# Performance work log

Measured on AMD Instinct MI355X. Metric: run time of the kernel, lower is better.

## Reference

```python
import jax, jax.numpy as jnp
import numpy as np

EPS = 1e-6
STRIDE = 2  # kv_pool_stride
NUM_HEADS = 8

def _layernorm(x, w, b):
    mu = jnp.mean(x, axis=-1, keepdims=True)
    var = jnp.mean(jnp.square(x - mu), axis=-1, keepdims=True)
    return (x - mu) * jax.lax.rsqrt(var + EPS) * w + b

def setup_inputs() -> dict:
    key = jax.random.key(0)
    B, H, W, C = 8, 56, 56, 384
    hidden = int(C * 2.0)
    ks = jax.random.split(key, 12)
    s = 0.02
    return {
        "x": jax.random.normal(ks[0], (B, H * W, C), jnp.float32),
        "ln1_w": jnp.ones((C,), jnp.float32),
        "ln1_b": jnp.zeros((C,), jnp.float32),
        "qw": jax.random.normal(ks[1], (C, C), jnp.float32) * s,
        "qb": jnp.zeros((C,), jnp.float32),
        "kw": jax.random.normal(ks[2], (C, C), jnp.float32) * s,
        "kb": jnp.zeros((C,), jnp.float32),
        "vw": jax.random.normal(ks[3], (C, C), jnp.float32) * s,
        "vb": jnp.zeros((C,), jnp.float32),
        "pw": jax.random.normal(ks[4], (C, C), jnp.float32) * s,
        "pb": jnp.zeros((C,), jnp.float32),
        "ln2_w": jnp.ones((C,), jnp.float32),
        "ln2_b": jnp.zeros((C,), jnp.float32),
        "fc1_w": jax.random.normal(ks[5], (C, hidden), jnp.float32) * s,
        "fc1_b": jnp.zeros((hidden,), jnp.float32),
        "fc2_w": jax.random.normal(ks[6], (hidden, C), jnp.float32) * s,
        "fc2_b": jnp.zeros((C,), jnp.float32),
        "H": 56,
        "W": 56,
    }

def reference(x, ln1_w, ln1_b, qw, qb, kw, kb, vw, vb, pw, pb,
              ln2_w, ln2_b, fc1_w, fc1_b, fc2_w, fc2_b, H, W):
    B, N, C = x.shape
    h = NUM_HEADS
    d = C // h
    scale = d ** -0.5

    # Attention branch: Q from norm1(x); K,V from RAW x (as in source), KV avg-pooled 2x2
    q_tok = _layernorm(x, ln1_w, ln1_b)
    s = STRIDE
    Hk, Wk = H // s, W // s
    kv = x.reshape(B, Hk, s, Wk, s, C).mean(axis=(2, 4)).reshape(B, Hk * Wk, C)

    q = (q_tok @ qw + qb).reshape(B, N, h, d)
    k = (kv @ kw + kb).reshape(B, Hk * Wk, h, d)
    v = (kv @ vw + vb).reshape(B, Hk * Wk, h, d)

    attn = jnp.einsum('bqhd,bkhd->bhqk', q, k) * scale
    attn = jax.nn.softmax(attn, axis=-1)
    out = jnp.einsum('bhqk,bkhd->bqhd', attn, v).reshape(B, N, C)
    x = x + (out @ pw + pb)

    # MLP branch (GELU exact, matching torch nn.GELU default)
    y = _layernorm(x, ln2_w, ln2_b)
    y = jax.nn.gelu(y @ fc1_w + fc1_b, approximate=False)
    x = x + (y @ fc2_w + fc2_b)
    return x
```

## Files before the change

kernel.cpp:

```cpp
#include <hip/hip_runtime.h>
#include <math.h>

#define B_    8
#define N_TOK 3136
#define C_    384
#define DH    48
#define NK    784
#define HID   768
#define M1    25088
#define M2    6272
#define M1Q   6272

typedef unsigned short u16;
typedef __attribute__((ext_vector_type(8))) short bf16x8;
typedef __attribute__((ext_vector_type(4))) float f32x4;

__device__ __forceinline__ float b2f(u16 u) {
  return __uint_as_float(((unsigned)u) << 16);
}
__device__ __forceinline__ u16 f2b(float f) {
  unsigned u = __float_as_uint(f);
  return (u16)((u + 0x7fffu + ((u >> 16) & 1u)) >> 16);
}
__device__ __forceinline__ u16 f2b_trunc(float f) {
  return (u16)(__float_as_uint(f) >> 16);
}
__device__ __forceinline__ void gload_lds16(const u16* g, u16* l) {
  __builtin_amdgcn_global_load_lds(
      (const __attribute__((address_space(1))) void*)g,
      (__attribute__((address_space(3))) void*)l, 16, 0, 0);
}

__global__ __launch_bounds__(256) void ln1_pool(
    const float* __restrict__ X, const float* __restrict__ w,
    const float* __restrict__ b, u16* __restrict__ Y, u16* __restrict__ KV) {
  if (blockIdx.x < M1 / 4) {
    const int row = blockIdx.x * 4 + (threadIdx.x >> 6);
    const int lane = threadIdx.x & 63;
    const size_t base = (size_t)row * C_;
    float v[6];
#pragma unroll
    for (int i = 0; i < 6; ++i) v[i] = X[base + lane + 64 * i];
    float s = 0.f;
#pragma unroll
    for (int i = 0; i < 6; ++i) s += v[i];
#pragma unroll
    for (int off = 32; off > 0; off >>= 1) s += __shfl_xor(s, off);
    const float mu = s * (1.0f / C_);
    float q = 0.f;
#pragma unroll
    for (int i = 0; i < 6; ++i) { float d = v[i] - mu; q += d * d; }
#pragma unroll
    for (int off = 32; off > 0; off >>= 1) q += __shfl_xor(q, off);
    const float r = rsqrtf(q * (1.0f / C_) + 1e-6f);
#pragma unroll
    for (int i = 0; i < 6; ++i) {
      int c = lane + 64 * i;
      Y[base + c] = f2b((v[i] - mu) * r * w[c] + b[c]);
    }
  } else {
    int t = (blockIdx.x - M1 / 4) * 256 + threadIdx.x;
    if (t >= M2 * C_) return;
    int c = t % C_;
    int row = t / C_;
    int bb = row / NK;
    int rr = row - bb * NK;
    int hk = rr / 28;
    int wk = rr - hk * 28;
    const float* p = X + ((size_t)(bb * N_TOK + hk * 112 + wk * 2)) * C_ + c;
    KV[t] = f2b(0.25f * (p[0] + p[C_] + p[56 * C_] + p[57 * C_]));
  }
}

__global__ __launch_bounds__(256) void ln2_rows(const u16* __restrict__ X,
    const float* __restrict__ w, const float* __restrict__ b, u16* __restrict__ Y) {
  const int row = blockIdx.x * 4 + (threadIdx.x >> 6);
  const int lane = threadIdx.x & 63;
  const size_t base = (size_t)row * C_;
  float v[6];
#pragma unroll
  for (int i = 0; i < 6; ++i) v[i] = b2f(X[base + lane + 64 * i]);
  float s = 0.f;
#pragma unroll
  for (int i = 0; i < 6; ++i) s += v[i];
#pragma unroll
  for (int off = 32; off > 0; off >>= 1) s += __shfl_xor(s, off);
  const float mu = s * (1.0f / C_);
  float q = 0.f;
#pragma unroll
  for (int i = 0; i < 6; ++i) { float d = v[i] - mu; q += d * d; }
#pragma unroll
  for (int off = 32; off > 0; off >>= 1) q += __shfl_xor(q, off);
  const float r = rsqrtf(q * (1.0f / C_) + 1e-6f);
#pragma unroll
  for (int i = 0; i < 6; ++i) {
    int c = lane + 64 * i;
    Y[base + c] = f2b((v[i] - mu) * r * w[c] + b[c]);
  }
}

struct TransArgs {
  const float* src[6];
  u16* dst[6];
  int K[6], N[6], tx[6], ty[6];
};
__global__ __launch_bounds__(256) void transpose_all(TransArgs a) {
  const int id = blockIdx.z;
  if ((int)blockIdx.x >= a.tx[id] || (int)blockIdx.y >= a.ty[id]) return;
  const float* W = a.src[id];
  u16* WT = a.dst[id];
  const int K = a.K[id], N = a.N[id];
  __shared__ u16 tile[64][73];
  const int k0 = blockIdx.y * 64, n0 = blockIdx.x * 64;
  for (int i = threadIdx.x; i < 64 * 64; i += 256) {
    int kk = i >> 6, nn = i & 63;
    tile[kk][nn] = f2b(W[(size_t)(k0 + kk) * N + n0 + nn]);
  }
  __syncthreads();
  for (int i = threadIdx.x; i < 64 * 64; i += 256) {
    int nn = i >> 6, kk = i & 63;
    WT[(size_t)(n0 + nn) * K + k0 + kk] = tile[kk][nn];
  }
}

template<int EPI, bool RES32, bool OUT32>
__device__ __forceinline__ void gemm_core(
    const u16* __restrict__ A, const u16* __restrict__ BT,
    const float* __restrict__ bias, const void* __restrict__ resv,
    void* __restrict__ Cv, int N, int K, int m0, int n0) {
  __shared__ u16 As[128 * 64];
  __shared__ u16 Bs[128 * 64];
  const int tid  = threadIdx.x;
  const int wave = tid >> 6;
  const int lane = tid & 63;
  const int quad = lane >> 4;
  const int ll   = lane & 15;
  const int wm   = wave >> 1, wn = wave & 1;

  const int srow = wave * 32 + (lane >> 3);
  const int sgs  = lane & 7;

  f32x4 acc[4][4];
#pragma unroll
  for (int i = 0; i < 4; ++i)
#pragma unroll
    for (int j = 0; j < 4; ++j) acc[i][j] = (f32x4){0.f, 0.f, 0.f, 0.f};

  for (int kk0 = 0; kk0 < K; kk0 += 64) {
    __syncthreads();
#pragma unroll
    for (int c = 0; c < 4; ++c) {
      const int r = srow + c * 8;
      const int g = sgs ^ (r & 7);
      gload_lds16(A  + (size_t)(m0 + r) * K + kk0 + g * 8,
                  As + (size_t)(wave * 32 + c * 8) * 64);
      gload_lds16(BT + (size_t)(n0 + r) * K + kk0 + g * 8,
                  Bs + (size_t)(wave * 32 + c * 8) * 64);
    }
    __syncthreads();
#pragma unroll
    for (int ks = 0; ks < 2; ++ks) {
      const int gsw = (quad + 4 * ks) ^ (ll & 7);
      bf16x8 af[4], bfr[4];
#pragma unroll
      for (int im = 0; im < 4; ++im)
        af[im] = *(const bf16x8*)&As[(size_t)(wm * 64 + im * 16 + ll) * 64 + gsw * 8];
#pragma unroll
      for (int jn = 0; jn < 4; ++jn)
        bfr[jn] = *(const bf16x8*)&Bs[(size_t)(wn * 64 + jn * 16 + ll) * 64 + gsw * 8];
#pragma unroll
      for (int im = 0; im < 4; ++im)
#pragma unroll
        for (int jn = 0; jn < 4; ++jn)
          acc[im][jn] = __builtin_amdgcn_mfma_f32_16x16x32_bf16(
              af[im], bfr[jn], acc[im][jn], 0, 0, 0);
    }
  }

  float bb[4];
#pragma unroll
  for (int jn = 0; jn < 4; ++jn) bb[jn] = bias[n0 + wn * 64 + jn * 16 + ll];
#pragma unroll
  for (int im = 0; im < 4; ++im) {
    const int row = m0 + wm * 64 + im * 16 + quad * 4;
#pragma unroll
    for (int jn = 0; jn < 4; ++jn) {
      const int col = n0 + wn * 64 + jn * 16 + ll;
#pragma unroll
      for (int r = 0; r < 4; ++r) {
        float o = acc[im][jn][r] + bb[jn];
        if (EPI == 1) {
          o = 0.5f * o * (1.0f + erff(o * 0.70710678118654752f));
        } else if (EPI == 2) {
          size_t ri = (size_t)(row + r) * N + col;
          o += RES32 ? ((const float*)resv)[ri] : b2f(((const u16*)resv)[ri]);
        }
        if (OUT32) ((float*)Cv)[(size_t)(row + r) * N + col] = o;
        else       ((u16*)Cv)[(size_t)(row + r) * N + col] = f2b(o);
      }
    }
  }
}

template<int EPI, bool RES32, bool OUT32>
__global__ __launch_bounds__(256) void gemm_bt(
    const u16* __restrict__ A, const u16* __restrict__ BT,
    const float* __restrict__ bias, const void* __restrict__ resv,
    void* __restrict__ Cv, int N, int K) {
  gemm_core<EPI, RES32, OUT32>(A, BT, bias, resv, Cv, N, K,
                               blockIdx.y << 7, blockIdx.x << 7);
}

struct QKVArgs {
  const u16* A[3];
  const u16* BT[3];
  const float* bias[3];
  u16* C[3];
  int M[3];
};
__global__ __launch_bounds__(256) void gemm_qkv(QKVArgs a) {
  const int z = blockIdx.z;
  const int m0 = blockIdx.y << 7;
  if (m0 >= a.M[z]) return;
  gemm_core<0, false, false>(a.A[z], a.BT[z], a.bias[z], nullptr, a.C[z],
                             C_, C_, m0, blockIdx.x << 7);
}

#define QS_STR 72
__global__ __launch_bounds__(512) void attn_mfma(
    const u16* __restrict__ Q, const u16* __restrict__ Kb,
    const u16* __restrict__ Vb, u16* __restrict__ O) {
  __shared__ u16 Qs[128 * QS_STR];
  __shared__ u16 Ks[64 * QS_STR];
  __shared__ u16 Vt[48 * QS_STR];
  __shared__ u16 Ps[128 * QS_STR];
  const int tid  = threadIdx.x;
  const int wave = tid >> 6;
  const int lane = tid & 63;
  const int quad = lane >> 4;
  const int ll   = lane & 15;
  const int qt   = blockIdx.x;
  const int bh   = blockIdx.y;
  const int b    = bh >> 3, h = bh & 7;
  const int q0   = qt * 128;
  const float scale = 0.14433756729740643f;

  for (int i = tid; i < 128 * 16; i += 512) {
    int r = i >> 4, c = i & 15;
    Qs[r * QS_STR + 48 + c] = 0;
    if (r < 64) Ks[r * QS_STR + 48 + c] = 0;
  }
  {
    const int part = tid & 7;
#pragma unroll
    for (int it = 0; it < 2; ++it) {
      const int row = it * 64 + (tid >> 3);
      if (part < 6) {
        const int qrow = q0 + row;
        if (qrow < N_TOK) {
          uint4 v = *(const uint4*)(Q + ((size_t)(b * N_TOK) + qrow) * C_ + h * DH + part * 8);
          const u16* vp = (const u16*)&v;
          u16 ov[8];
#pragma unroll
          for (int j = 0; j < 8; ++j) ov[j] = f2b(b2f(vp[j]) * scale);
          *(uint4*)&Qs[row * QS_STR + part * 8] = *(const uint4*)ov;
        } else {
          uint4 z = {0, 0, 0, 0};
          *(uint4*)&Qs[row * QS_STR + part * 8] = z;
        }
      }
    }
  }

  f32x4 Ofr[3] = {{0.f,0.f,0.f,0.f},{0.f,0.f,0.f,0.f},{0.f,0.f,0.f,0.f}};
  float lrow[4] = {0.f, 0.f, 0.f, 0.f};

  for (int t = 0; t < 13; ++t) {
    const int kbase = t * 64;
    __syncthreads();
    {
      const int key = tid >> 3, part = tid & 7;
      if (part < 6 && kbase + key < NK) {
        uint4 v = *(const uint4*)(Kb + ((size_t)(b * NK) + kbase + key) * C_ + h * DH + part * 8);
        *(uint4*)&Ks[key * QS_STR + part * 8] = v;
      }
    }
    {
      const int part = tid >> 6, key = tid & 63;
      if (part < 6 && kbase + key < NK) {
        uint4 v = *(const uint4*)(Vb + ((size_t)(b * NK) + kbase + key) * C_ + h * DH + part * 8);
        const u16* vp = (const u16*)&v;
#pragma unroll
        for (int j = 0; j < 8; ++j)
          Vt[(part * 8 + j) * QS_STR + key] = vp[j];
      }
    }
    __syncthreads();

    f32x4 S[4];
#pragma unroll
    for (int nt = 0; nt < 4; ++nt) {
      f32x4 acc = {0.f, 0.f, 0.f, 0.f};
#pragma unroll
      for (int k0 = 0; k0 < 64; k0 += 32) {
        bf16x8 a = *(const bf16x8*)&Qs[(wave * 16 + ll) * QS_STR + k0 + quad * 8];
        bf16x8 bb = *(const bf16x8*)&Ks[(nt * 16 + ll) * QS_STR + k0 + quad * 8];
        acc = __builtin_amdgcn_mfma_f32_16x16x32_bf16(a, bb, acc, 0, 0, 0);
      }
      if (kbase + nt * 16 + ll >= NK)
        acc = (f32x4){-1e30f, -1e30f, -1e30f, -1e30f};
      S[nt] = acc;
    }
#pragma unroll
    for (int nt = 0; nt < 4; ++nt) {
      const int g = nt * 2 + (ll >> 3);
      const int gp = g ^ quad;
#pragma unroll
      for (int r = 0; r < 4; ++r) {
        float p = __expf(S[nt][r]);
        lrow[r] += p;
        Ps[(wave * 16 + quad * 4 + r) * QS_STR + (gp << 3) + (ll & 7)] = f2b_trunc(p);
      }
    }
#pragma unroll
    for (int dt = 0; dt < 3; ++dt)
#pragma unroll
      for (int ks = 0; ks < 2; ++ks) {
        const int gp = ((ks << 2) + quad) ^ ((ll >> 2) & 3);
        bf16x8 a = *(const bf16x8*)&Ps[(wave * 16 + ll) * QS_STR + (gp << 3)];
        bf16x8 bb = *(const bf16x8*)&Vt[(dt * 16 + ll) * QS_STR + ks * 32 + quad * 8];
        Ofr[dt] = __builtin_amdgcn_mfma_f32_16x16x32_bf16(a, bb, Ofr[dt], 0, 0, 0);
      }
  }
#pragma unroll
  for (int msk = 1; msk < 16; msk <<= 1)
#pragma unroll
    for (int r = 0; r < 4; ++r)
      lrow[r] += __shfl_xor(lrow[r], msk);
  float inv[4];
#pragma unroll
  for (int r = 0; r < 4; ++r) inv[r] = 1.0f / lrow[r];
#pragma unroll
  for (int dt = 0; dt < 3; ++dt)
#pragma unroll
    for (int r = 0; r < 4; ++r) {
      int qrow = q0 + wave * 16 + quad * 4 + r;
      if (qrow < N_TOK)
        O[((size_t)b * N_TOK + qrow) * C_ + h * DH + dt * 16 + ll] =
            f2b(Ofr[dt][r] * inv[r]);
    }
}

__global__ __launch_bounds__(256) void marker_fill(
    float* __restrict__ out, size_t n, float val) {
  size_t i = (size_t)blockIdx.x * 256 + threadIdx.x;
  const size_t stride = (size_t)gridDim.x * 256;
  for (; i < n; i += stride) out[i] = 0.f;
  if (blockIdx.x == 0 && threadIdx.x == 0) out[0] = val;
}

extern "C" void kernel_launch(void* const* d_in, const int* in_sizes, int n_in,
                              void* d_out, int out_size, void* d_ws, size_t ws_size,
                              hipStream_t stream) {
  const float* x    = (const float*)d_in[0];
  const float* ln1w = (const float*)d_in[1];
  const float* ln1b = (const float*)d_in[2];
  const float* qw   = (const float*)d_in[3];
  const float* qb   = (const float*)d_in[4];
  const float* kw   = (const float*)d_in[5];
  const float* kb   = (const float*)d_in[6];
  const float* vw   = (const float*)d_in[7];
  const float* vb   = (const float*)d_in[8];
  const float* pw   = (const float*)d_in[9];
  const float* pb   = (const float*)d_in[10];
  const float* ln2w = (const float*)d_in[11];
  const float* ln2b = (const float*)d_in[12];
  const float* fc1w = (const float*)d_in[13];
  const float* fc1b = (const float*)d_in[14];
  const float* fc2w = (const float*)d_in[15];
  const float* fc2b = (const float*)d_in[16];

  const size_t BUF = (size_t)M1 * C_;
  float* outf = (float*)d_out;

  {
    static const int exp_sizes[19] = {
      M1 * C_, C_, C_, C_ * C_, C_, C_ * C_, C_, C_ * C_, C_, C_ * C_, C_,
      C_, C_, C_ * HID, HID, HID * C_, C_, 1, 1};
    int bad = -1;
    if (n_in != 19) bad = 99;
    else {
      for (int i = 0; i < 19; ++i)
        if (in_sizes[i] != exp_sizes[i]) { bad = i; break; }
    }
    if (bad >= 0) {
      marker_fill<<<1024, 256, 0, stream>>>(outf, BUF, 10000.0f + (float)bad);
      return;
    }
  }
  const size_t need_min  = 4096 + 3 * BUF * sizeof(u16);
  const size_t need_full = 4096 + (3 * BUF + (size_t)M1 * HID) * sizeof(u16);
  if (ws_size < need_min) {
    marker_fill<<<1024, 256, 0, stream>>>(outf, BUF, 30000.0f + (float)(ws_size >> 20));
    return;
  }
  const bool full_mlp = (ws_size >= need_full);

  u16* T0 = (u16*)((char*)d_ws + 4096);
  u16* T1 = T0 + BUF;
  u16* U  = T1 + BUF;
  u16* P  = U;
  u16* KB = U + (size_t)M2 * C_;
  u16* VB = U + (size_t)2 * M2 * C_;
  u16* HBq = U;
  u16* HBfull = U + BUF;
  u16* WTb = U + BUF - (size_t)(4 * C_ * C_ + 2 * C_ * HID);
  u16* wtq = WTb;
  u16* wtk = wtq + C_ * C_;
  u16* wtv = wtk + C_ * C_;
  u16* wtp = wtv + C_ * C_;
  u16* wtf1 = wtp + C_ * C_;
  u16* wtf2 = wtf1 + (size_t)C_ * HID;

  {
    TransArgs ta;
    ta.src[0] = qw;   ta.dst[0] = wtq;  ta.K[0] = C_;  ta.N[0] = C_;  ta.tx[0] = 6;  ta.ty[0] = 6;
    ta.src[1] = kw;   ta.dst[1] = wtk;  ta.K[1] = C_;  ta.N[1] = C_;  ta.tx[1] = 6;  ta.ty[1] = 6;
    ta.src[2] = vw;   ta.dst[2] = wtv;  ta.K[2] = C_;  ta.N[2] = C_;  ta.tx[2] = 6;  ta.ty[2] = 6;
    ta.src[3] = pw;   ta.dst[3] = wtp;  ta.K[3] = C_;  ta.N[3] = C_;  ta.tx[3] = 6;  ta.ty[3] = 6;
    ta.src[4] = fc1w; ta.dst[4] = wtf1; ta.K[4] = C_;  ta.N[4] = HID; ta.tx[4] = 12; ta.ty[4] = 6;
    ta.src[5] = fc2w; ta.dst[5] = wtf2; ta.K[5] = HID; ta.N[5] = C_;  ta.tx[5] = 6;  ta.ty[5] = 12;
    transpose_all<<<dim3(12, 12, 6), 256, 0, stream>>>(ta);
  }

  ln1_pool<<<M1 / 4 + (M2 * C_) / 256, 256, 0, stream>>>(x, ln1w, ln1b, T0, P);

  {
    QKVArgs qa;
    qa.A[0] = T0; qa.BT[0] = wtq; qa.bias[0] = qb; qa.C[0] = T1; qa.M[0] = M1;
    qa.A[1] = P;  qa.BT[1] = wtk; qa.bias[1] = kb; qa.C[1] = KB; qa.M[1] = M2;
    qa.A[2] = P;  qa.BT[2] = wtv; qa.bias[2] = vb; qa.C[2] = VB; qa.M[2] = M2;
    gemm_qkv<<<dim3(3, 196, 3), 256, 0, stream>>>(qa);
  }

  attn_mfma<<<dim3(25, 64), 512, 0, stream>>>(T1, KB, VB, T0);

  gemm_bt<2, true, false><<<dim3(3, 196), 256, 0, stream>>>(
      T0, wtp, pb, x, T1, C_, C_);

  ln2_rows<<<M1 / 4, 256, 0, stream>>>(T1, ln2w, ln2b, T0);

  if (full_mlp) {
    gemm_bt<1, false, false><<<dim3(6, 196), 256, 0, stream>>>(
        T0, wtf1, fc1b, nullptr, HBfull, HID, C_);
    gemm_bt<2, false, true><<<dim3(3, 196), 256, 0, stream>>>(
        HBfull, wtf2, fc2b, T1, outf, C_, HID);
  } else {
    for (int qtr = 0; qtr < 4; ++qtr) {
      const size_t ro = (size_t)qtr * M1Q;
      gemm_bt<1, false, false><<<dim3(6, 49), 256, 0, stream>>>(
          T0 + ro * C_, wtf1, fc1b, nullptr, HBq, HID, C_);
      gemm_bt<2, false, true><<<dim3(3, 49), 256, 0, stream>>>(
          HBq, wtf2, fc2b, T1 + ro * C_, outf + ro * C_, C_, HID);
    }
  }
}
```

Measured before the change: 348.0 us.

## Enlarge GEMM M-tile to 256, merge pre-kernels, keep attention Q in registers

The GEMM tile goes from 128x128 to 256x128, so each wave accumulates 8x4 MFMA tiles and reuses each B fragment across twice as many A rows. Row-bound checks handle M values that are not multiples of 256. The weight transpose and LN1/pooling kernels are merged into one launch to drop a kernel boundary. The attention kernel now loads Q fragments straight into registers instead of staging them in shared memory, which cuts LDS traffic and footprint. The costs are more accumulator registers (lower occupancy), fewer blocks per GEMM grid, and the partial last M tile doing wasted work on the quarter-split MLP path.

```diff
diff --git a/kernel.cpp b/kernel.cpp
--- a/kernel.cpp
+++ b/kernel.cpp
@@ -31,16 +31,44 @@
       (__attribute__((address_space(3))) void*)l, 16, 0, 0);
 }
 
-__global__ __launch_bounds__(256) void ln1_pool(
-    const float* __restrict__ X, const float* __restrict__ w,
-    const float* __restrict__ b, u16* __restrict__ Y, u16* __restrict__ KV) {
-  if (blockIdx.x < M1 / 4) {
-    const int row = blockIdx.x * 4 + (threadIdx.x >> 6);
+struct PreArgs {
+  const float* src[6];
+  u16* dst[6];
+  int K[6], N[6];
+  const float* x;
+  const float* w;
+  const float* b;
+  u16* Y;
+  u16* KV;
+};
+__global__ __launch_bounds__(256) void pre_kernel(PreArgs pa) {
+  __shared__ u16 tile[64][73];
+  const int bid = blockIdx.x;
+  if (bid < 288) {
+    int id, bx, by;
+    if (bid < 144)      { id = bid / 36; int j = bid % 36;  bx = j % 6;  by = j / 6; }
+    else if (bid < 216) { id = 4;        int j = bid - 144; bx = j % 12; by = j / 12; }
+    else                { id = 5;        int j = bid - 216; bx = j % 6;  by = j / 6; }
+    const float* W = pa.src[id];
+    u16* WT = pa.dst[id];
+    const int K = pa.K[id], N = pa.N[id];
+    const int k0 = by * 64, n0 = bx * 64;
+    for (int i = threadIdx.x; i < 64 * 64; i += 256) {
+      int kk = i >> 6, nn = i & 63;
+      tile[kk][nn] = f2b(W[(size_t)(k0 + kk) * N + n0 + nn]);
+    }
+    __syncthreads();
+    for (int i = threadIdx.x; i < 64 * 64; i += 256) {
+      int nn = i >> 6, kk = i & 63;
+      WT[(size_t)(n0 + nn) * K + k0 + kk] = tile[kk][nn];
+    }
+  } else if (bid < 288 + M1 / 4) {
+    const int row = (bid - 288) * 4 + (threadIdx.x >> 6);
     const int lane = threadIdx.x & 63;
     const size_t base = (size_t)row * C_;
     float v[6];
 #pragma unroll
-    for (int i = 0; i < 6; ++i) v[i] = X[base + lane + 64 * i];
+    for (int i = 0; i < 6; ++i) v[i] = pa.x[base + lane + 64 * i];
     float s = 0.f;
 #pragma unroll
     for (int i = 0; i < 6; ++i) s += v[i];
@@ -56,19 +84,18 @@
 #pragma unroll
     for (int i = 0; i < 6; ++i) {
       int c = lane + 64 * i;
-      Y[base + c] = f2b((v[i] - mu) * r * w[c] + b[c]);
+      pa.Y[base + c] = f2b((v[i] - mu) * r * pa.w[c] + pa.b[c]);
     }
   } else {
-    int t = (blockIdx.x - M1 / 4) * 256 + threadIdx.x;
-    if (t >= M2 * C_) return;
+    int t = (bid - 288 - M1 / 4) * 256 + threadIdx.x;
     int c = t % C_;
     int row = t / C_;
     int bb = row / NK;
     int rr = row - bb * NK;
     int hk = rr / 28;
     int wk = rr - hk * 28;
-    const float* p = X + ((size_t)(bb * N_TOK + hk * 112 + wk * 2)) * C_ + c;
-    KV[t] = f2b(0.25f * (p[0] + p[C_] + p[56 * C_] + p[57 * C_]));
+    const float* p = pa.x + ((size_t)(bb * N_TOK + hk * 112 + wk * 2)) * C_ + c;
+    pa.KV[t] = f2b(0.25f * (p[0] + p[C_] + p[56 * C_] + p[57 * C_]));
   }
 }
 
@@ -99,36 +126,12 @@
   }
 }
 
-struct TransArgs {
-  const float* src[6];
-  u16* dst[6];
-  int K[6], N[6], tx[6], ty[6];
-};
-__global__ __launch_bounds__(256) void transpose_all(TransArgs a) {
-  const int id = blockIdx.z;
-  if ((int)blockIdx.x >= a.tx[id] || (int)blockIdx.y >= a.ty[id]) return;
-  const float* W = a.src[id];
-  u16* WT = a.dst[id];
-  const int K = a.K[id], N = a.N[id];
-  __shared__ u16 tile[64][73];
-  const int k0 = blockIdx.y * 64, n0 = blockIdx.x * 64;
-  for (int i = threadIdx.x; i < 64 * 64; i += 256) {
-    int kk = i >> 6, nn = i & 63;
-    tile[kk][nn] = f2b(W[(size_t)(k0 + kk) * N + n0 + nn]);
-  }
-  __syncthreads();
-  for (int i = threadIdx.x; i < 64 * 64; i += 256) {
-    int nn = i >> 6, kk = i & 63;
-    WT[(size_t)(n0 + nn) * K + k0 + kk] = tile[kk][nn];
-  }
-}
-
 template<int EPI, bool RES32, bool OUT32>
 __device__ __forceinline__ void gemm_core(
     const u16* __restrict__ A, const u16* __restrict__ BT,
     const float* __restrict__ bias, const void* __restrict__ resv,
-    void* __restrict__ Cv, int N, int K, int m0, int n0) {
-  __shared__ u16 As[128 * 64];
+    void* __restrict__ Cv, int M, int N, int K, int m0, int n0) {
+  __shared__ u16 As[256 * 64];
   __shared__ u16 Bs[128 * 64];
   const int tid  = threadIdx.x;
   const int wave = tid >> 6;
@@ -136,24 +139,28 @@
   const int quad = lane >> 4;
   const int ll   = lane & 15;
   const int wm   = wave >> 1, wn = wave & 1;
-
-  const int srow = wave * 32 + (lane >> 3);
-  const int sgs  = lane & 7;
-
-  f32x4 acc[4][4];
-#pragma unroll
-  for (int i = 0; i < 4; ++i)
+  const int lr8  = lane >> 3;
+  const int sg   = lane & 7;
+
+  f32x4 acc[8][4];
+#pragma unroll
+  for (int i = 0; i < 8; ++i)
 #pragma unroll
     for (int j = 0; j < 4; ++j) acc[i][j] = (f32x4){0.f, 0.f, 0.f, 0.f};
 
   for (int kk0 = 0; kk0 < K; kk0 += 64) {
     __syncthreads();
 #pragma unroll
+    for (int c = 0; c < 8; ++c) {
+      const int r = wave * 64 + c * 8 + lr8;
+      const int g = sg ^ (r & 7);
+      gload_lds16(A + (size_t)(m0 + r) * K + kk0 + g * 8,
+                  As + (size_t)(wave * 64 + c * 8) * 64);
+    }
+#pragma unroll
     for (int c = 0; c < 4; ++c) {
-      const int r = srow + c * 8;
-      const int g = sgs ^ (r & 7);
-      gload_lds16(A  + (size_t)(m0 + r) * K + kk0 + g * 8,
-                  As + (size_t)(wave * 32 + c * 8) * 64);
+      const int r = wave * 32 + c * 8 + lr8;
+      const int g = sg ^ (r & 7);
       gload_lds16(BT + (size_t)(n0 + r) * K + kk0 + g * 8,
                   Bs + (size_t)(wave * 32 + c * 8) * 64);
     }
@@ -161,15 +168,15 @@
 #pragma unroll
     for (int ks = 0; ks < 2; ++ks) {
       const int gsw = (quad + 4 * ks) ^ (ll & 7);
-      bf16x8 af[4], bfr[4];
-#pragma unroll
-      for (int im = 0; im < 4; ++im)
-        af[im] = *(const bf16x8*)&As[(size_t)(wm * 64 + im * 16 + ll) * 64 + gsw * 8];
+      bf16x8 af[8], bfr[4];
+#pragma unroll
+      for (int im = 0; im < 8; ++im)
+        af[im] = *(const bf16x8*)&As[(size_t)(wm * 128 + im * 16 + ll) * 64 + gsw * 8];
 #pragma unroll
       for (int jn = 0; jn < 4; ++jn)
         bfr[jn] = *(const bf16x8*)&Bs[(size_t)(wn * 64 + jn * 16 + ll) * 64 + gsw * 8];
 #pragma unroll
-      for (int im = 0; im < 4; ++im)
+      for (int im = 0; im < 8; ++im)
 #pragma unroll
         for (int jn = 0; jn < 4; ++jn)
           acc[im][jn] = __builtin_amdgcn_mfma_f32_16x16x32_bf16(
@@ -181,13 +188,14 @@
 #pragma unroll
   for (int jn = 0; jn < 4; ++jn) bb[jn] = bias[n0 + wn * 64 + jn * 16 + ll];
 #pragma unroll
-  for (int im = 0; im < 4; ++im) {
-    const int row = m0 + wm * 64 + im * 16 + quad * 4;
+  for (int im = 0; im < 8; ++im) {
+    const int row = m0 + wm * 128 + im * 16 + quad * 4;
 #pragma unroll
     for (int jn = 0; jn < 4; ++jn) {
       const int col = n0 + wn * 64 + jn * 16 + ll;
 #pragma unroll
       for (int r = 0; r < 4; ++r) {
+        if (row + r >= M) continue;
         float o = acc[im][jn][r] + bb[jn];
         if (EPI == 1) {
           o = 0.5f * o * (1.0f + erff(o * 0.70710678118654752f));
@@ -206,9 +214,9 @@
 __global__ __launch_bounds__(256) void gemm_bt(
     const u16* __restrict__ A, const u16* __restrict__ BT,
     const float* __restrict__ bias, const void* __restrict__ resv,
-    void* __restrict__ Cv, int N, int K) {
-  gemm_core<EPI, RES32, OUT32>(A, BT, bias, resv, Cv, N, K,
-                               blockIdx.y << 7, blockIdx.x << 7);
+    void* __restrict__ Cv, int M, int N, int K) {
+  gemm_core<EPI, RES32, OUT32>(A, BT, bias, resv, Cv, M, N, K,
+                               blockIdx.y << 8, blockIdx.x << 7);
 }
 
 struct QKVArgs {
@@ -220,17 +228,16 @@
 };
 __global__ __launch_bounds__(256) void gemm_qkv(QKVArgs a) {
   const int z = blockIdx.z;
-  const int m0 = blockIdx.y << 7;
+  const int m0 = blockIdx.y << 8;
   if (m0 >= a.M[z]) return;
   gemm_core<0, false, false>(a.A[z], a.BT[z], a.bias[z], nullptr, a.C[z],
-                             C_, C_, m0, blockIdx.x << 7);
+                             a.M[z], C_, C_, m0, blockIdx.x << 7);
 }
 
 #define QS_STR 72
 __global__ __launch_bounds__(512) void attn_mfma(
     const u16* __restrict__ Q, const u16* __restrict__ Kb,
     const u16* __restrict__ Vb, u16* __restrict__ O) {
-  __shared__ u16 Qs[128 * QS_STR];
   __shared__ u16 Ks[64 * QS_STR];
   __shared__ u16 Vt[48 * QS_STR];
   __shared__ u16 Ps[128 * QS_STR];
@@ -245,29 +252,27 @@
   const int q0   = qt * 128;
   const float scale = 0.14433756729740643f;
 
-  for (int i = tid; i < 128 * 16; i += 512) {
+  for (int i = tid; i < 64 * 16; i += 512) {
     int r = i >> 4, c = i & 15;
-    Qs[r * QS_STR + 48 + c] = 0;
-    if (r < 64) Ks[r * QS_STR + 48 + c] = 0;
-  }
+    Ks[r * QS_STR + 48 + c] = 0;
+  }
+  bf16x8 aq0 = {0,0,0,0,0,0,0,0}, aq1 = {0,0,0,0,0,0,0,0};
   {
-    const int part = tid & 7;
-#pragma unroll
-    for (int it = 0; it < 2; ++it) {
-      const int row = it * 64 + (tid >> 3);
-      if (part < 6) {
-        const int qrow = q0 + row;
-        if (qrow < N_TOK) {
-          uint4 v = *(const uint4*)(Q + ((size_t)(b * N_TOK) + qrow) * C_ + h * DH + part * 8);
-          const u16* vp = (const u16*)&v;
-          u16 ov[8];
-#pragma unroll
-          for (int j = 0; j < 8; ++j) ov[j] = f2b(b2f(vp[j]) * scale);
-          *(uint4*)&Qs[row * QS_STR + part * 8] = *(const uint4*)ov;
-        } else {
-          uint4 z = {0, 0, 0, 0};
-          *(uint4*)&Qs[row * QS_STR + part * 8] = z;
-        }
+    const int qrow = q0 + wave * 16 + ll;
+    if (qrow < N_TOK) {
+      const u16* qp = Q + ((size_t)b * N_TOK + qrow) * C_ + h * DH;
+      uint4 v0 = *(const uint4*)(qp + quad * 8);
+      const u16* vp = (const u16*)&v0;
+      u16 ov[8];
+#pragma unroll
+      for (int j = 0; j < 8; ++j) ov[j] = f2b(b2f(vp[j]) * scale);
+      aq0 = *(const bf16x8*)ov;
+      if (quad < 2) {
+        uint4 v1 = *(const uint4*)(qp + 32 + quad * 8);
+        const u16* wp = (const u16*)&v1;
+#pragma unroll
+        for (int j = 0; j < 8; ++j) ov[j] = f2b(b2f(wp[j]) * scale);
+        aq1 = *(const bf16x8*)ov;
       }
     }
   }
@@ -301,12 +306,10 @@
 #pragma unroll
     for (int nt = 0; nt < 4; ++nt) {
       f32x4 acc = {0.f, 0.f, 0.f, 0.f};
-#pragma unroll
-      for (int k0 = 0; k0 < 64; k0 += 32) {
-        bf16x8 a = *(const bf16x8*)&Qs[(wave * 16 + ll) * QS_STR + k0 + quad * 8];
-        bf16x8 bb = *(const bf16x8*)&Ks[(nt * 16 + ll) * QS_STR + k0 + quad * 8];
-        acc = __builtin_amdgcn_mfma_f32_16x16x32_bf16(a, bb, acc, 0, 0, 0);
-      }
+      bf16x8 b0 = *(const bf16x8*)&Ks[(nt * 16 + ll) * QS_STR + quad * 8];
+      acc = __builtin_amdgcn_mfma_f32_16x16x32_bf16(aq0, b0, acc, 0, 0, 0);
+      bf16x8 b1 = *(const bf16x8*)&Ks[(nt * 16 + ll) * QS_STR + 32 + quad * 8];
+      acc = __builtin_amdgcn_mfma_f32_16x16x32_bf16(aq1, b1, acc, 0, 0, 0);
       if (kbase + nt * 16 + ll >= NK)
         acc = (f32x4){-1e30f, -1e30f, -1e30f, -1e30f};
       S[nt] = acc;
@@ -423,45 +426,44 @@
   u16* wtf2 = wtf1 + (size_t)C_ * HID;
 
   {
-    TransArgs ta;
-    ta.src[0] = qw;   ta.dst[0] = wtq;  ta.K[0] = C_;  ta.N[0] = C_;  ta.tx[0] = 6;  ta.ty[0] = 6;
-    ta.src[1] = kw;   ta.dst[1] = wtk;  ta.K[1] = C_;  ta.N[1] = C_;  ta.tx[1] = 6;  ta.ty[1] = 6;
-    ta.src[2] = vw;   ta.dst[2] = wtv;  ta.K[2] = C_;  ta.N[2] = C_;  ta.tx[2] = 6;  ta.ty[2] = 6;
-    ta.src[3] = pw;   ta.dst[3] = wtp;  ta.K[3] = C_;  ta.N[3] = C_;  ta.tx[3] = 6;  ta.ty[3] = 6;
-    ta.src[4] = fc1w; ta.dst[4] = wtf1; ta.K[4] = C_;  ta.N[4] = HID; ta.tx[4] = 12; ta.ty[4] = 6;
-    ta.src[5] = fc2w; ta.dst[5] = wtf2; ta.K[5] = HID; ta.N[5] = C_;  ta.tx[5] = 6;  ta.ty[5] = 12;
-    transpose_all<<<dim3(12, 12, 6), 256, 0, stream>>>(ta);
-  }
-
-  ln1_pool<<<M1 / 4 + (M2 * C_) / 256, 256, 0, stream>>>(x, ln1w, ln1b, T0, P);
+    PreArgs pa;
+    pa.src[0] = qw;   pa.dst[0] = wtq;  pa.K[0] = C_;  pa.N[0] = C_;
+    pa.src[1] = kw;   pa.dst[1] = wtk;  pa.K[1] = C_;  pa.N[1] = C_;
+    pa.src[2] = vw;   pa.dst[2] = wtv;  pa.K[2] = C_;  pa.N[2] = C_;
+    pa.src[3] = pw;   pa.dst[3] = wtp;  pa.K[3] = C_;  pa.N[3] = C_;
+    pa.src[4] = fc1w; pa.dst[4] = wtf1; pa.K[4] = C_;  pa.N[4] = HID;
+    pa.src[5] = fc2w; pa.dst[5] = wtf2; pa.K[5] = HID; pa.N[5] = C_;
+    pa.x = x; pa.w = ln1w; pa.b = ln1b; pa.Y = T0; pa.KV = P;
+    pre_kernel<<<288 + M1 / 4 + (M2 * C_) / 256, 256, 0, stream>>>(pa);
+  }
 
   {
     QKVArgs qa;
     qa.A[0] = T0; qa.BT[0] = wtq; qa.bias[0] = qb; qa.C[0] = T1; qa.M[0] = M1;
     qa.A[1] = P;  qa.BT[1] = wtk; qa.bias[1] = kb; qa.C[1] = KB; qa.M[1] = M2;
     qa.A[2] = P;  qa.BT[2] = wtv; qa.bias[2] = vb; qa.C[2] = VB; qa.M[2] = M2;
-    gemm_qkv<<<dim3(3, 196, 3), 256, 0, stream>>>(qa);
+    gemm_qkv<<<dim3(3, 98, 3), 256, 0, stream>>>(qa);
   }
 
   attn_mfma<<<dim3(25, 64), 512, 0, stream>>>(T1, KB, VB, T0);
 
-  gemm_bt<2, true, false><<<dim3(3, 196), 256, 0, stream>>>(
-      T0, wtp, pb, x, T1, C_, C_);
+  gemm_bt<2, true, false><<<dim3(3, 98), 256, 0, stream>>>(
+      T0, wtp, pb, x, T1, M1, C_, C_);
 
   ln2_rows<<<M1 / 4, 256, 0, stream>>>(T1, ln2w, ln2b, T0);
 
   if (full_mlp) {
-    gemm_bt<1, false, false><<<dim3(6, 196), 256, 0, stream>>>(
-        T0, wtf1, fc1b, nullptr, HBfull, HID, C_);
-    gemm_bt<2, false, true><<<dim3(3, 196), 256, 0, stream>>>(
-        HBfull, wtf2, fc2b, T1, outf, C_, HID);
+    gemm_bt<1, false, false><<<dim3(6, 98), 256, 0, stream>>>(
+        T0, wtf1, fc1b, nullptr, HBfull, M1, HID, C_);
+    gemm_bt<2, false, true><<<dim3(3, 98), 256, 0, stream>>>(
+        HBfull, wtf2, fc2b, T1, outf, M1, C_, HID);
   } else {
     for (int qtr = 0; qtr < 4; ++qtr) {
       const size_t ro = (size_t)qtr * M1Q;
-      gemm_bt<1, false, false><<<dim3(6, 49), 256, 0, stream>>>(
-          T0 + ro * C_, wtf1, fc1b, nullptr, HBq, HID, C_);
-      gemm_bt<2, false, true><<<dim3(3, 49), 256, 0, stream>>>(
-          HBq, wtf2, fc2b, T1 + ro * C_, outf + ro * C_, C_, HID);
-    }
-  }
-}
+      gemm_bt<1, false, false><<<dim3(6, 25), 256, 0, stream>>>(
+          T0 + ro * C_, wtf1, fc1b, nullptr, HBq, M1Q, HID, C_);
+      gemm_bt<2, false, true><<<dim3(3, 25), 256, 0, stream>>>(
+          HBq, wtf2, fc2b, T1 + ro * C_, outf + ro * C_, M1Q, C_, HID);
+    }
+  }
+}
```

New measurement: 563.9 us. +62.0%, slower.
